# Performance work log

Hardware: AMD Instinct MI355X
Metric: run time of the kernel (lower is better)

Reference implementation:

```python
import jax, jax.numpy as jnp
import numpy as np

D_MODEL = 1024
NUM_HEADS = 16
D_K = D_MODEL // NUM_HEADS  # 64
THETA = 10000.0


def setup_inputs() -> dict:
    key = jax.random.key(0)
    k_x, k_q, k_k, k_v, k_o = jax.random.split(key, 5)
    B, S = 2, 2048
    std = (2.0 / (D_MODEL + D_MODEL)) ** 0.5
    x = jax.random.normal(k_x, (B, S, D_MODEL), dtype=jnp.float32)
    Wq = std * jax.random.truncated_normal(k_q, -3.0, 3.0, (D_MODEL, D_MODEL), dtype=jnp.float32)
    Wk = std * jax.random.truncated_normal(k_k, -3.0, 3.0, (D_MODEL, D_MODEL), dtype=jnp.float32)
    Wv = std * jax.random.truncated_normal(k_v, -3.0, 3.0, (D_MODEL, D_MODEL), dtype=jnp.float32)
    Wo = std * jax.random.truncated_normal(k_o, -3.0, 3.0, (D_MODEL, D_MODEL), dtype=jnp.float32)
    return {"x": x, "Wq": Wq, "Wk": Wk, "Wv": Wv, "Wo": Wo}


def _apply_rope(t, cos, sin):
    # t: [B, H, S, d_k]; cos/sin: [S, d_k//2] broadcast over B, H
    tr = t.reshape(*t.shape[:-1], D_K // 2, 2)
    t1, t2 = tr[..., 0], tr[..., 1]
    r1 = t1 * cos - t2 * sin
    r2 = t1 * sin + t2 * cos
    return jnp.stack([r1, r2], axis=-1).reshape(t.shape)


def reference(x, Wq, Wk, Wv, Wo):
    B, S, D = x.shape
    H, dk = NUM_HEADS, D_K
    # projections (no bias): y = x @ W.T
    Q = (x @ Wq.T).reshape(B, S, H, dk).transpose(0, 2, 1, 3)  # [B,H,S,dk]
    K = (x @ Wk.T).reshape(B, S, H, dk).transpose(0, 2, 1, 3)
    V = (x @ Wv.T).reshape(B, S, H, dk).transpose(0, 2, 1, 3)
    # RoPE angles for positions 0..S-1
    pos = jnp.arange(S, dtype=jnp.float32)[:, None]            # [S,1]
    freqs = 1.0 / (THETA ** (jnp.arange(0, dk, 2, dtype=jnp.float32) / dk))  # [dk/2]
    angles = pos * freqs[None, :]                              # [S, dk/2]
    cos, sin = jnp.cos(angles), jnp.sin(angles)
    Q = _apply_rope(Q, cos, sin)
    K = _apply_rope(K, cos, sin)
    # causal scaled dot-product attention
    scores = jnp.einsum("bhqd,bhkd->bhqk", Q, K) / jnp.sqrt(jnp.float32(dk))
    causal = jnp.tril(jnp.ones((S, S), dtype=bool))
    scores = jnp.where(causal, scores, -jnp.inf)
    probs = jax.nn.softmax(scores, axis=-1)
    attn = jnp.einsum("bhqk,bhkd->bhqd", probs, V)             # [B,H,S,dk]
    attn = attn.transpose(0, 2, 1, 3).reshape(B, S, H * dk)
    return attn @ Wo.T
```

## Files before the change

### kernel.cpp

```cpp
#include <hip/hip_runtime.h>
#include <hip/hip_bf16.h>

typedef __bf16 bf16;
typedef __bf16 bf16x8 __attribute__((ext_vector_type(8)));
typedef float f32x4 __attribute__((ext_vector_type(4)));

#define MFMA16(A, B, C) __builtin_amdgcn_mfma_f32_16x16x32_bf16((A), (B), (C), 0, 0, 0)

static __device__ __forceinline__ void gload16(const bf16* g, bf16* l) {
    __builtin_amdgcn_global_load_lds((const __attribute__((address_space(1))) void*)g,
                                     (__attribute__((address_space(3))) void*)l, 16, 0, 0);
}

__global__ void detect_kernel(const void* w, int* flag) {
    float v = (float)((const bf16*)w)[threadIdx.x];
    unsigned long long bad = __ballot(!(fabsf(v) < 1.0f));
    if (threadIdx.x == 0) *flag = bad ? 1 : 0;
}

__global__ __launch_bounds__(256) void convert_all(const void* x, const void* w0,
                                                   const void* w1, const void* w2,
                                                   const void* w3, bf16* xb, bf16* b0,
                                                   bf16* b1, bf16* b2, bf16* b3,
                                                   const int* flagp) {
    if (*flagp == 0) return;
    int id = (blockIdx.x * 256 + threadIdx.x) * 4;
    const int XN = 1 << 22;
    const float* src;
    bf16* dst;
    int off;
    if (id < XN) {
        src = (const float*)x; dst = xb; off = id;
    } else {
        int r = id - XN;
        int wi = r >> 20;
        off = r & ((1 << 20) - 1);
        src = (const float*)(wi == 0 ? w0 : wi == 1 ? w1 : wi == 2 ? w2 : w3);
        dst = (wi == 0 ? b0 : wi == 1 ? b1 : wi == 2 ? b2 : b3);
    }
    float4 v = *(const float4*)(src + off);
    bf16 o[4] = {(bf16)v.x, (bf16)v.y, (bf16)v.z, (bf16)v.w};
    *(uint2*)(dst + off) = *(uint2*)o;
}

template <int MODE>
__global__ __launch_bounds__(256) void gemm128(const void* rawA, const bf16* convA,
                                               const void* rW0, const bf16* cW0,
                                               const void* rW1, const bf16* cW1,
                                               const void* rW2, const bf16* cW2,
                                               bf16* Qo, bf16* Ko, bf16* Vt,
                                               void* Cout, const int* flagp) {
    const int K = 1024;
    __shared__ __attribute__((aligned(16))) bf16 lsA[128 * 64];
    __shared__ __attribute__((aligned(16))) bf16 lsB[128 * 64];
    const int flag = *flagp;
    const bf16* A = flag ? convA : (const bf16*)rawA;
    int tensor, n0;
    const bf16* W;
    if (MODE == 0) {
        tensor = blockIdx.x >> 3;
        n0 = (blockIdx.x & 7) * 128;
        W = tensor == 0 ? (flag ? cW0 : (const bf16*)rW0)
          : tensor == 1 ? (flag ? cW1 : (const bf16*)rW1)
                        : (flag ? cW2 : (const bf16*)rW2);
    } else {
        tensor = 0;
        n0 = blockIdx.x * 128;
        W = flag ? cW0 : (const bf16*)rW0;
    }
    const int t = threadIdx.x;
    const int m0 = blockIdx.y * 128;
    const int w = t >> 6, lane = t & 63;
    const int wr = w >> 1, wc = w & 1;
    const int llo = lane & 15, quad = lane >> 4;

    const int srow = t >> 3;
    const int sc = (t & 7) ^ (srow & 7);
    const bf16* Ab = A + (size_t)(m0 + srow) * K + sc * 8;
    const bf16* Wb = W + (size_t)(n0 + srow) * K + sc * 8;
    bf16* lA = &lsA[t * 8];
    bf16* lB = &lsB[t * 8];

    f32x4 acc[4][4] = {};

    for (int k0 = 0; k0 < K; k0 += 64) {
#pragma unroll
        for (int j = 0; j < 4; ++j) gload16(Ab + (size_t)j * 32 * K + k0, lA + j * 2048);
#pragma unroll
        for (int j = 0; j < 4; ++j) gload16(Wb + (size_t)j * 32 * K + k0, lB + j * 2048);
        __syncthreads();
#pragma unroll
        for (int kc = 0; kc < 2; ++kc) {
            bf16x8 a[4], bb[4];
            const int g = kc * 4 + quad;
#pragma unroll
            for (int mi = 0; mi < 4; ++mi) {
                int r = wr * 64 + mi * 16 + llo;
                a[mi] = *(const bf16x8*)&lsA[r * 64 + ((g ^ (r & 7)) * 8)];
            }
#pragma unroll
            for (int ni = 0; ni < 4; ++ni) {
                int r = wc * 64 + ni * 16 + llo;
                bb[ni] = *(const bf16x8*)&lsB[r * 64 + ((g ^ (r & 7)) * 8)];
            }
#pragma unroll
            for (int mi = 0; mi < 4; ++mi)
#pragma unroll
                for (int ni = 0; ni < 4; ++ni)
                    acc[mi][ni] = MFMA16(a[mi], bb[ni], acc[mi][ni]);
        }
        __syncthreads();
    }

#pragma unroll
    for (int mi = 0; mi < 4; ++mi)
#pragma unroll
        for (int ni = 0; ni < 4; ++ni)
#pragma unroll
            for (int r = 0; r < 4; ++r) {
                int row = m0 + wr * 64 + mi * 16 + quad * 4 + r;
                int col = n0 + wc * 64 + ni * 16 + llo;
                float v = acc[mi][ni][r];
                if (MODE == 1) {
                    if (flag)
                        ((float*)Cout)[(size_t)row * 1024 + col] = v;
                    else
                        ((bf16*)Cout)[(size_t)row * 1024 + col] = (bf16)v;
                } else if (tensor == 2) {
                    int b = row >> 11, s = row & 2047;
                    Vt[((size_t)b * 1024 + col) * 2048 + s] = (bf16)v;
                } else {
                    int d = col & 63, s = row & 2047;
                    float partner = __shfl_xor(v, 1);
                    float freq = exp2f((float)(d >> 1) * -0.4152410118609203f);
                    float rev = (float)s * freq * 0.15915494309189535f;
                    rev -= floorf(rev);
                    float sn = __builtin_amdgcn_sinf(rev);
                    float cs = __builtin_amdgcn_cosf(rev);
                    float outv = v * cs + partner * sn * ((d & 1) ? 1.0f : -1.0f);
                    bf16* dst = (tensor == 0) ? Qo : Ko;
                    dst[(size_t)row * 1024 + col] = (bf16)outv;
                }
            }
}

__global__ __launch_bounds__(256) void attn_kernel(const bf16* __restrict__ Q,
                                                   const bf16* __restrict__ Kr,
                                                   const bf16* __restrict__ Vt,
                                                   bf16* __restrict__ O) {
    __shared__ __attribute__((aligned(16))) bf16 lsK[64 * 64];
    __shared__ __attribute__((aligned(16))) bf16 lsV[64 * 64];
    __shared__ __attribute__((aligned(16))) bf16 lsP[4][32 * 72];
    const int blk = blockIdx.x;
    const int ib = 15 - (blk >> 5);
    const int bh = blk & 31;
    const int b = bh >> 4, h = bh & 15;
    const int t = threadIdx.x, w = t >> 6, lane = t & 63;
    const int llo = lane & 15, quad = lane >> 4;
    const int Q0 = ib * 128, q0w = Q0 + w * 32;

    bf16x8 aQ[2][2];
#pragma unroll
    for (int qi = 0; qi < 2; ++qi) {
        const size_t qb = ((size_t)(b * 2048 + q0w + qi * 16 + llo)) * 1024 + h * 64 + quad * 8;
        aQ[qi][0] = *(const bf16x8*)&Q[qb];
        aQ[qi][1] = *(const bf16x8*)&Q[qb + 32];
    }

    f32x4 o[2][4] = {};
    float lpart[2] = {0.f, 0.f};
    const float SC = 0.18033688011112042f;
    const int qlane0 = q0w + llo;

    const int srow8 = lane >> 3;
    const int sc = (lane & 7) ^ srow8;
    const int nch = 2 * ib + 2;

    for (int tt = 0; tt < nch; ++tt) {
        const int kv0 = tt * 64;
#pragma unroll
        for (int jj = 0; jj < 2; ++jj) {
            int seg = w + jj * 4;
            int rowk = seg * 8 + srow8;
            gload16(&Kr[((size_t)(b * 2048 + kv0 + rowk)) * 1024 + h * 64 + sc * 8],
                    &lsK[seg * 512 + lane * 8]);
            gload16(&Vt[((size_t)(b * 1024 + h * 64 + rowk)) * 2048 + kv0 + sc * 8],
                    &lsV[seg * 512 + lane * 8]);
        }
        __syncthreads();

        if (kv0 <= q0w + 31) {
            const bool need_mask = (kv0 + 63 >= q0w);
#pragma unroll
            for (int qi = 0; qi < 2; ++qi) {
                const int q = qlane0 + qi * 16;
#pragma unroll
                for (int half = 0; half < 4; ++half) {
                    int rk = half * 16 + llo;
                    bf16x8 k0 = *(const bf16x8*)&lsK[rk * 64 + ((quad ^ (rk & 7)) * 8)];
                    bf16x8 k1 = *(const bf16x8*)&lsK[rk * 64 + (((quad + 4) ^ (rk & 7)) * 8)];
                    f32x4 z = {};
                    z = MFMA16(k0, aQ[qi][0], z);
                    z = MFMA16(k1, aQ[qi][1], z);
                    union { bf16 hh[4]; uint2 u; } pk;
                    if (need_mask) {
                        int kvb = kv0 + half * 16 + quad * 4;
#pragma unroll
                        for (int r = 0; r < 4; ++r) {
                            float e = (kvb + r <= q) ? z[r] * SC : -INFINITY;
                            float p = exp2f(e);
                            lpart[qi] += p;
                            pk.hh[r] = (bf16)p;
                        }
                    } else {
#pragma unroll
                        for (int r = 0; r < 4; ++r) {
                            float p = exp2f(z[r] * SC);
                            lpart[qi] += p;
                            pk.hh[r] = (bf16)p;
                        }
                    }
                    *(uint2*)&lsP[w][(qi * 16 + llo) * 72 + half * 16 + quad * 4] = pk.u;
                }
            }
            __builtin_amdgcn_wave_barrier();
#pragma unroll
            for (int qi = 0; qi < 2; ++qi)
#pragma unroll
                for (int kc = 0; kc < 2; ++kc) {
                    bf16x8 aP =
                        *(const bf16x8*)&lsP[w][(qi * 16 + llo) * 72 + kc * 32 + quad * 8];
#pragma unroll
                    for (int g = 0; g < 4; ++g) {
                        int rv = g * 16 + llo;
                        int cg = kc * 4 + quad;
                        bf16x8 bV = *(const bf16x8*)&lsV[rv * 64 + ((cg ^ (rv & 7)) * 8)];
                        o[qi][g] = MFMA16(aP, bV, o[qi][g]);
                    }
                }
            __builtin_amdgcn_wave_barrier();
        }
        __syncthreads();
    }

    float lfull[2];
#pragma unroll
    for (int qi = 0; qi < 2; ++qi) {
        float l = lpart[qi];
        l += __shfl_xor(l, 16);
        l += __shfl_xor(l, 32);
        lfull[qi] = l;
    }
#pragma unroll
    for (int qi = 0; qi < 2; ++qi)
#pragma unroll
        for (int r = 0; r < 4; ++r) {
            float l = __shfl(lfull[qi], (lane & 48) | (quad * 4 + r));
            float inv = 1.f / l;
            int q = q0w + qi * 16 + quad * 4 + r;
            size_t ob = ((size_t)(b * 2048 + q)) * 1024 + h * 64;
#pragma unroll
            for (int g = 0; g < 4; ++g)
                O[ob + g * 16 + llo] = (bf16)(o[qi][g][r] * inv);
        }
}

extern "C" void kernel_launch(void* const* d_in, const int* in_sizes, int n_in,
                              void* d_out, int out_size, void* d_ws, size_t ws_size,
                              hipStream_t stream) {
    const size_t TN = (size_t)4096 * 1024;

    int* flag = (int*)d_ws;
    bf16* Q = (bf16*)((char*)d_ws + 256);
    bf16* Kb = Q + TN;
    bf16* Vt = Kb + TN;
    bf16* xb = Vt + TN;
    bf16* Wb0 = xb + TN;
    bf16* Wb1 = Wb0 + TN / 4;
    bf16* Wb2 = Wb1 + TN / 4;
    bf16* Wb3 = Wb2 + TN / 4;
    bf16* AO = Q;

    detect_kernel<<<1, 64, 0, stream>>>(d_in[1], flag);
    convert_all<<<8192, 256, 0, stream>>>(d_in[0], d_in[1], d_in[2], d_in[3], d_in[4],
                                          xb, Wb0, Wb1, Wb2, Wb3, flag);

    gemm128<0><<<dim3(24, 32), 256, 0, stream>>>(d_in[0], xb, d_in[1], Wb0, d_in[2],
                                                 Wb1, d_in[3], Wb2, Q, Kb, Vt, nullptr,
                                                 flag);

    attn_kernel<<<512, 256, 0, stream>>>(Q, Kb, Vt, AO);

    gemm128<1><<<dim3(8, 32), 256, 0, stream>>>(AO, AO, d_in[4], Wb3, nullptr, nullptr,
                                                nullptr, nullptr, nullptr, nullptr,
                                                nullptr, d_out, flag);
}
```

Measured before the change: 227.9 us.

## Double-buffer attention K/V tiles, rebalance schedule, and split output GEMM into narrower tiles

The attention kernel now double-buffers K and V tiles in LDS, prefetching the next chunk while computing the current one, so one barrier per iteration is dropped. K and V fragments are hoisted into registers, and the P buffer uses an XOR swizzle instead of padding. Query blocks are interleaved heavy and light to balance causal work. The output projection gets its own 128x64-tile kernel, giving 512 blocks instead of 256 for better CU occupancy, at the cost of more LDS per attention block and higher register pressure.

After: 215.4 us. -5.5%, faster.

```diff
diff --git a/kernel.cpp b/kernel.cpp
--- a/kernel.cpp
+++ b/kernel.cpp
@@ -43,31 +43,22 @@
     *(uint2*)(dst + off) = *(uint2*)o;
 }
 
-template <int MODE>
-__global__ __launch_bounds__(256) void gemm128(const void* rawA, const bf16* convA,
-                                               const void* rW0, const bf16* cW0,
-                                               const void* rW1, const bf16* cW1,
-                                               const void* rW2, const bf16* cW2,
-                                               bf16* Qo, bf16* Ko, bf16* Vt,
-                                               void* Cout, const int* flagp) {
+__global__ __launch_bounds__(256) void gemm_qkv(const void* rawA, const bf16* convA,
+                                                const void* rW0, const bf16* cW0,
+                                                const void* rW1, const bf16* cW1,
+                                                const void* rW2, const bf16* cW2,
+                                                bf16* Qo, bf16* Ko, bf16* Vt,
+                                                const int* flagp) {
     const int K = 1024;
     __shared__ __attribute__((aligned(16))) bf16 lsA[128 * 64];
     __shared__ __attribute__((aligned(16))) bf16 lsB[128 * 64];
     const int flag = *flagp;
     const bf16* A = flag ? convA : (const bf16*)rawA;
-    int tensor, n0;
-    const bf16* W;
-    if (MODE == 0) {
-        tensor = blockIdx.x >> 3;
-        n0 = (blockIdx.x & 7) * 128;
-        W = tensor == 0 ? (flag ? cW0 : (const bf16*)rW0)
-          : tensor == 1 ? (flag ? cW1 : (const bf16*)rW1)
-                        : (flag ? cW2 : (const bf16*)rW2);
-    } else {
-        tensor = 0;
-        n0 = blockIdx.x * 128;
-        W = flag ? cW0 : (const bf16*)rW0;
-    }
+    const int tensor = blockIdx.x >> 3;
+    const int n0 = (blockIdx.x & 7) * 128;
+    const bf16* W = tensor == 0 ? (flag ? cW0 : (const bf16*)rW0)
+                  : tensor == 1 ? (flag ? cW1 : (const bf16*)rW1)
+                                : (flag ? cW2 : (const bf16*)rW2);
     const int t = threadIdx.x;
     const int m0 = blockIdx.y * 128;
     const int w = t >> 6, lane = t & 63;
@@ -121,12 +112,7 @@
                 int row = m0 + wr * 64 + mi * 16 + quad * 4 + r;
                 int col = n0 + wc * 64 + ni * 16 + llo;
                 float v = acc[mi][ni][r];
-                if (MODE == 1) {
-                    if (flag)
-                        ((float*)Cout)[(size_t)row * 1024 + col] = v;
-                    else
-                        ((bf16*)Cout)[(size_t)row * 1024 + col] = (bf16)v;
-                } else if (tensor == 2) {
+                if (tensor == 2) {
                     int b = row >> 11, s = row & 2047;
                     Vt[((size_t)b * 1024 + col) * 2048 + s] = (bf16)v;
                 } else {
@@ -144,25 +130,94 @@
             }
 }
 
-__global__ __launch_bounds__(256) void attn_kernel(const bf16* __restrict__ Q,
-                                                   const bf16* __restrict__ Kr,
-                                                   const bf16* __restrict__ Vt,
-                                                   bf16* __restrict__ O) {
-    __shared__ __attribute__((aligned(16))) bf16 lsK[64 * 64];
-    __shared__ __attribute__((aligned(16))) bf16 lsV[64 * 64];
-    __shared__ __attribute__((aligned(16))) bf16 lsP[4][32 * 72];
+__global__ __launch_bounds__(256) void gemm_out(const bf16* A, const void* rW,
+                                                const bf16* cW, void* Cout,
+                                                const int* flagp) {
+    const int K = 1024;
+    __shared__ __attribute__((aligned(16))) bf16 lsA[128 * 64];
+    __shared__ __attribute__((aligned(16))) bf16 lsB[64 * 64];
+    const int flag = *flagp;
+    const bf16* W = flag ? cW : (const bf16*)rW;
+    const int t = threadIdx.x;
+    const int m0 = blockIdx.y * 128;
+    const int n0 = blockIdx.x * 64;
+    const int w = t >> 6, lane = t & 63;
+    const int llo = lane & 15, quad = lane >> 4;
+    const int srow = t >> 3;
+    const int sc = (t & 7) ^ (srow & 7);
+    const bf16* Ab = A + (size_t)(m0 + srow) * K + sc * 8;
+    const bf16* Wb = W + (size_t)(n0 + srow) * K + sc * 8;
+    bf16* lA = &lsA[t * 8];
+    bf16* lB = &lsB[t * 8];
+
+    f32x4 acc[2][4] = {};
+
+    for (int k0 = 0; k0 < K; k0 += 64) {
+#pragma unroll
+        for (int j = 0; j < 4; ++j) gload16(Ab + (size_t)j * 32 * K + k0, lA + j * 2048);
+#pragma unroll
+        for (int j = 0; j < 2; ++j) gload16(Wb + (size_t)j * 32 * K + k0, lB + j * 2048);
+        __syncthreads();
+#pragma unroll
+        for (int kc = 0; kc < 2; ++kc) {
+            bf16x8 a[2], bb[4];
+            const int g = kc * 4 + quad;
+#pragma unroll
+            for (int mi = 0; mi < 2; ++mi) {
+                int r = w * 32 + mi * 16 + llo;
+                a[mi] = *(const bf16x8*)&lsA[r * 64 + ((g ^ (r & 7)) * 8)];
+            }
+#pragma unroll
+            for (int ni = 0; ni < 4; ++ni) {
+                int r = ni * 16 + llo;
+                bb[ni] = *(const bf16x8*)&lsB[r * 64 + ((g ^ (r & 7)) * 8)];
+            }
+#pragma unroll
+            for (int mi = 0; mi < 2; ++mi)
+#pragma unroll
+                for (int ni = 0; ni < 4; ++ni)
+                    acc[mi][ni] = MFMA16(a[mi], bb[ni], acc[mi][ni]);
+        }
+        __syncthreads();
+    }
+
+#pragma unroll
+    for (int mi = 0; mi < 2; ++mi)
+#pragma unroll
+        for (int ni = 0; ni < 4; ++ni)
+#pragma unroll
+            for (int r = 0; r < 4; ++r) {
+                int row = m0 + w * 32 + mi * 16 + quad * 4 + r;
+                int col = n0 + ni * 16 + llo;
+                float v = acc[mi][ni][r];
+                if (flag)
+                    ((float*)Cout)[(size_t)row * 1024 + col] = v;
+                else
+                    ((bf16*)Cout)[(size_t)row * 1024 + col] = (bf16)v;
+            }
+}
+
+__global__ __launch_bounds__(256, 2) void attn_kernel(const bf16* __restrict__ Q,
+                                                      const bf16* __restrict__ Kr,
+                                                      const bf16* __restrict__ Vt,
+                                                      bf16* __restrict__ O) {
+    __shared__ __attribute__((aligned(16))) bf16 lsK[2][64 * 64];
+    __shared__ __attribute__((aligned(16))) bf16 lsV[2][64 * 64];
+    __shared__ __attribute__((aligned(16))) bf16 lsP[4][32 * 64];
     const int blk = blockIdx.x;
-    const int ib = 15 - (blk >> 5);
+    const int u = blk >> 5;
+    const int ib = (u < 8) ? (15 - u) : (u - 8);
     const int bh = blk & 31;
     const int b = bh >> 4, h = bh & 15;
     const int t = threadIdx.x, w = t >> 6, lane = t & 63;
     const int llo = lane & 15, quad = lane >> 4;
-    const int Q0 = ib * 128, q0w = Q0 + w * 32;
+    const int q0w = ib * 128 + w * 32;
 
     bf16x8 aQ[2][2];
 #pragma unroll
     for (int qi = 0; qi < 2; ++qi) {
-        const size_t qb = ((size_t)(b * 2048 + q0w + qi * 16 + llo)) * 1024 + h * 64 + quad * 8;
+        const size_t qb =
+            ((size_t)(b * 2048 + q0w + qi * 16 + llo)) * 1024 + h * 64 + quad * 8;
         aQ[qi][0] = *(const bf16x8*)&Q[qb];
         aQ[qi][1] = *(const bf16x8*)&Q[qb + 32];
     }
@@ -176,33 +231,58 @@
     const int sc = (lane & 7) ^ srow8;
     const int nch = 2 * ib + 2;
 
-    for (int tt = 0; tt < nch; ++tt) {
+    auto stage = [&](int tt, int buf) {
         const int kv0 = tt * 64;
 #pragma unroll
         for (int jj = 0; jj < 2; ++jj) {
             int seg = w + jj * 4;
             int rowk = seg * 8 + srow8;
             gload16(&Kr[((size_t)(b * 2048 + kv0 + rowk)) * 1024 + h * 64 + sc * 8],
-                    &lsK[seg * 512 + lane * 8]);
+                    &lsK[buf][seg * 512 + lane * 8]);
             gload16(&Vt[((size_t)(b * 1024 + h * 64 + rowk)) * 2048 + kv0 + sc * 8],
-                    &lsV[seg * 512 + lane * 8]);
-        }
-        __syncthreads();
+                    &lsV[buf][seg * 512 + lane * 8]);
+        }
+    };
+
+    stage(0, 0);
+
+    for (int tt = 0; tt < nch; ++tt) {
+        const int cur = tt & 1;
+        const int kv0 = tt * 64;
+        __syncthreads();
+        if (tt + 1 < nch) stage(tt + 1, cur ^ 1);
 
         if (kv0 <= q0w + 31) {
+            bf16x8 kf[4][2];
+#pragma unroll
+            for (int half = 0; half < 4; ++half) {
+                int rk = half * 16 + llo;
+                kf[half][0] = *(const bf16x8*)&lsK[cur][rk * 64 + ((quad ^ (rk & 7)) * 8)];
+                kf[half][1] =
+                    *(const bf16x8*)&lsK[cur][rk * 64 + (((quad + 4) ^ (rk & 7)) * 8)];
+            }
+            bf16x8 vf[2][4];
+#pragma unroll
+            for (int kc = 0; kc < 2; ++kc)
+#pragma unroll
+                for (int g = 0; g < 4; ++g) {
+                    int rv = g * 16 + llo;
+                    int cg = kc * 4 + quad;
+                    vf[kc][g] =
+                        *(const bf16x8*)&lsV[cur][rv * 64 + ((cg ^ (rv & 7)) * 8)];
+                }
+
             const bool need_mask = (kv0 + 63 >= q0w);
 #pragma unroll
             for (int qi = 0; qi < 2; ++qi) {
                 const int q = qlane0 + qi * 16;
+                const int prow = qi * 16 + llo;
 #pragma unroll
                 for (int half = 0; half < 4; ++half) {
-                    int rk = half * 16 + llo;
-                    bf16x8 k0 = *(const bf16x8*)&lsK[rk * 64 + ((quad ^ (rk & 7)) * 8)];
-                    bf16x8 k1 = *(const bf16x8*)&lsK[rk * 64 + (((quad + 4) ^ (rk & 7)) * 8)];
                     f32x4 z = {};
-                    z = MFMA16(k0, aQ[qi][0], z);
-                    z = MFMA16(k1, aQ[qi][1], z);
-                    union { bf16 hh[4]; uint2 u; } pk;
+                    z = MFMA16(kf[half][0], aQ[qi][0], z);
+                    z = MFMA16(kf[half][1], aQ[qi][1], z);
+                    union { bf16 hh[4]; uint2 uu; } pk;
                     if (need_mask) {
                         int kvb = kv0 + half * 16 + quad * 4;
 #pragma unroll
@@ -220,27 +300,26 @@
                             pk.hh[r] = (bf16)p;
                         }
                     }
-                    *(uint2*)&lsP[w][(qi * 16 + llo) * 72 + half * 16 + quad * 4] = pk.u;
+                    int cw = 2 * half + (quad >> 1);
+                    *(uint2*)&lsP[w][prow * 64 + ((cw ^ (llo & 7)) * 8) + (quad & 1) * 4] =
+                        pk.uu;
                 }
             }
             __builtin_amdgcn_wave_barrier();
 #pragma unroll
-            for (int qi = 0; qi < 2; ++qi)
+            for (int qi = 0; qi < 2; ++qi) {
+                const int prow = qi * 16 + llo;
 #pragma unroll
                 for (int kc = 0; kc < 2; ++kc) {
+                    int cr = 4 * kc + quad;
                     bf16x8 aP =
-                        *(const bf16x8*)&lsP[w][(qi * 16 + llo) * 72 + kc * 32 + quad * 8];
-#pragma unroll
-                    for (int g = 0; g < 4; ++g) {
-                        int rv = g * 16 + llo;
-                        int cg = kc * 4 + quad;
-                        bf16x8 bV = *(const bf16x8*)&lsV[rv * 64 + ((cg ^ (rv & 7)) * 8)];
-                        o[qi][g] = MFMA16(aP, bV, o[qi][g]);
-                    }
+                        *(const bf16x8*)&lsP[w][prow * 64 + ((cr ^ (llo & 7)) * 8)];
+#pragma unroll
+                    for (int g = 0; g < 4; ++g) o[qi][g] = MFMA16(aP, vf[kc][g], o[qi][g]);
                 }
+            }
             __builtin_amdgcn_wave_barrier();
         }
-        __syncthreads();
     }
 
     float lfull[2];
@@ -285,13 +364,10 @@
     convert_all<<<8192, 256, 0, stream>>>(d_in[0], d_in[1], d_in[2], d_in[3], d_in[4],
                                           xb, Wb0, Wb1, Wb2, Wb3, flag);
 
-    gemm128<0><<<dim3(24, 32), 256, 0, stream>>>(d_in[0], xb, d_in[1], Wb0, d_in[2],
-                                                 Wb1, d_in[3], Wb2, Q, Kb, Vt, nullptr,
-                                                 flag);
+    gemm_qkv<<<dim3(24, 32), 256, 0, stream>>>(d_in[0], xb, d_in[1], Wb0, d_in[2], Wb1,
+                                               d_in[3], Wb2, Q, Kb, Vt, flag);
 
     attn_kernel<<<512, 256, 0, stream>>>(Q, Kb, Vt, AO);
 
-    gemm128<1><<<dim3(8, 32), 256, 0, stream>>>(AO, AO, d_in[4], Wb3, nullptr, nullptr,
-                                                nullptr, nullptr, nullptr, nullptr,
-                                                nullptr, d_out, flag);
-}
+    gemm_out<<<dim3(16, 32), 256, 0, stream>>>(AO, d_in[4], Wb3, d_out, flag);
+}
```

## Double-buffer LDS in GEMM and attention, shrink GEMM tiles, balance causal blocks

Applied to the files above, without the earlier changes.

The GEMM moves to 128x64 tiles with 128 threads and a 32-wide K step, and double-buffers LDS so the next tile's global-to-LDS load overlaps the current tile's MFMAs. The attention kernel double-buffers K/V tiles, drops the trailing syncthreads, hoists K and V fragment reads out of the inner loops, swizzles the P scratch, and reorders query blocks so long and short causal rows interleave. The aim is to hide global load latency, raise occupancy and balance work across CUs. In exchange it holds more registers for the hoisted fragments and uses twice the shared memory in attention.

After: 224.3 us. About the same (-1.5%).

```diff
diff --git a/kernel.cpp b/kernel.cpp
--- a/kernel.cpp
+++ b/kernel.cpp
@@ -44,72 +44,82 @@
 }
 
 template <int MODE>
-__global__ __launch_bounds__(256) void gemm128(const void* rawA, const bf16* convA,
-                                               const void* rW0, const bf16* cW0,
-                                               const void* rW1, const bf16* cW1,
-                                               const void* rW2, const bf16* cW2,
-                                               bf16* Qo, bf16* Ko, bf16* Vt,
-                                               void* Cout, const int* flagp) {
+__global__ __launch_bounds__(128, 3) void gemm_nt(const void* rawA, const bf16* convA,
+                                                  const void* rW0, const bf16* cW0,
+                                                  const void* rW1, const bf16* cW1,
+                                                  const void* rW2, const bf16* cW2,
+                                                  bf16* Qo, bf16* Ko, bf16* Vt,
+                                                  void* Cout, const int* flagp) {
     const int K = 1024;
-    __shared__ __attribute__((aligned(16))) bf16 lsA[128 * 64];
-    __shared__ __attribute__((aligned(16))) bf16 lsB[128 * 64];
+    __shared__ __attribute__((aligned(16))) bf16 lsA[2][128 * 32];
+    __shared__ __attribute__((aligned(16))) bf16 lsB[2][64 * 32];
     const int flag = *flagp;
     const bf16* A = flag ? convA : (const bf16*)rawA;
     int tensor, n0;
     const bf16* W;
     if (MODE == 0) {
-        tensor = blockIdx.x >> 3;
-        n0 = (blockIdx.x & 7) * 128;
+        tensor = blockIdx.x >> 4;
+        n0 = (blockIdx.x & 15) * 64;
         W = tensor == 0 ? (flag ? cW0 : (const bf16*)rW0)
           : tensor == 1 ? (flag ? cW1 : (const bf16*)rW1)
                         : (flag ? cW2 : (const bf16*)rW2);
     } else {
         tensor = 0;
-        n0 = blockIdx.x * 128;
+        n0 = blockIdx.x * 64;
         W = flag ? cW0 : (const bf16*)rW0;
     }
     const int t = threadIdx.x;
     const int m0 = blockIdx.y * 128;
     const int w = t >> 6, lane = t & 63;
-    const int wr = w >> 1, wc = w & 1;
     const int llo = lane & 15, quad = lane >> 4;
-
-    const int srow = t >> 3;
-    const int sc = (t & 7) ^ (srow & 7);
-    const bf16* Ab = A + (size_t)(m0 + srow) * K + sc * 8;
-    const bf16* Wb = W + (size_t)(n0 + srow) * K + sc * 8;
-    bf16* lA = &lsA[t * 8];
-    bf16* lB = &lsB[t * 8];
+    const int sel = (llo >> 1) & 3;
 
     f32x4 acc[4][4] = {};
 
-    for (int k0 = 0; k0 < K; k0 += 64) {
-#pragma unroll
-        for (int j = 0; j < 4; ++j) gload16(Ab + (size_t)j * 32 * K + k0, lA + j * 2048);
-#pragma unroll
-        for (int j = 0; j < 4; ++j) gload16(Wb + (size_t)j * 32 * K + k0, lB + j * 2048);
+    auto stage = [&](int k0, int buf) {
+#pragma unroll
+        for (int j = 0; j < 4; ++j) {
+            int c = j * 128 + t;
+            int row = c >> 2, pos = c & 3;
+            int g = pos ^ ((row >> 1) & 3);
+            gload16(A + (size_t)(m0 + row) * K + k0 + g * 8, &lsA[buf][c * 8]);
+        }
+#pragma unroll
+        for (int j = 0; j < 2; ++j) {
+            int c = j * 128 + t;
+            int row = c >> 2, pos = c & 3;
+            int g = pos ^ ((row >> 1) & 3);
+            gload16(W + (size_t)(n0 + row) * K + k0 + g * 8, &lsB[buf][c * 8]);
+        }
+    };
+
+    auto compute = [&](int buf) {
+        bf16x8 a[4], bb[4];
+#pragma unroll
+        for (int mi = 0; mi < 4; ++mi) {
+            int r = w * 64 + mi * 16 + llo;
+            a[mi] = *(const bf16x8*)&lsA[buf][r * 32 + ((quad ^ sel) * 8)];
+        }
+#pragma unroll
+        for (int ni = 0; ni < 4; ++ni) {
+            int r = ni * 16 + llo;
+            bb[ni] = *(const bf16x8*)&lsB[buf][r * 32 + ((quad ^ sel) * 8)];
+        }
+#pragma unroll
+        for (int mi = 0; mi < 4; ++mi)
+#pragma unroll
+            for (int ni = 0; ni < 4; ++ni)
+                acc[mi][ni] = MFMA16(a[mi], bb[ni], acc[mi][ni]);
+    };
+
+    stage(0, 0);
+    for (int it = 0; it < 32; it += 2) {
         __syncthreads();
-#pragma unroll
-        for (int kc = 0; kc < 2; ++kc) {
-            bf16x8 a[4], bb[4];
-            const int g = kc * 4 + quad;
-#pragma unroll
-            for (int mi = 0; mi < 4; ++mi) {
-                int r = wr * 64 + mi * 16 + llo;
-                a[mi] = *(const bf16x8*)&lsA[r * 64 + ((g ^ (r & 7)) * 8)];
-            }
-#pragma unroll
-            for (int ni = 0; ni < 4; ++ni) {
-                int r = wc * 64 + ni * 16 + llo;
-                bb[ni] = *(const bf16x8*)&lsB[r * 64 + ((g ^ (r & 7)) * 8)];
-            }
-#pragma unroll
-            for (int mi = 0; mi < 4; ++mi)
-#pragma unroll
-                for (int ni = 0; ni < 4; ++ni)
-                    acc[mi][ni] = MFMA16(a[mi], bb[ni], acc[mi][ni]);
-        }
+        stage((it + 1) * 32, 1);
+        compute(0);
         __syncthreads();
+        if (it + 2 < 32) stage((it + 2) * 32, 0);
+        compute(1);
     }
 
 #pragma unroll
@@ -118,8 +128,8 @@
         for (int ni = 0; ni < 4; ++ni)
 #pragma unroll
             for (int r = 0; r < 4; ++r) {
-                int row = m0 + wr * 64 + mi * 16 + quad * 4 + r;
-                int col = n0 + wc * 64 + ni * 16 + llo;
+                int row = m0 + w * 64 + mi * 16 + quad * 4 + r;
+                int col = n0 + ni * 16 + llo;
                 float v = acc[mi][ni][r];
                 if (MODE == 1) {
                     if (flag)
@@ -144,25 +154,27 @@
             }
 }
 
-__global__ __launch_bounds__(256) void attn_kernel(const bf16* __restrict__ Q,
-                                                   const bf16* __restrict__ Kr,
-                                                   const bf16* __restrict__ Vt,
-                                                   bf16* __restrict__ O) {
-    __shared__ __attribute__((aligned(16))) bf16 lsK[64 * 64];
-    __shared__ __attribute__((aligned(16))) bf16 lsV[64 * 64];
-    __shared__ __attribute__((aligned(16))) bf16 lsP[4][32 * 72];
+__global__ __launch_bounds__(256, 2) void attn_kernel(const bf16* __restrict__ Q,
+                                                      const bf16* __restrict__ Kr,
+                                                      const bf16* __restrict__ Vt,
+                                                      bf16* __restrict__ O) {
+    __shared__ __attribute__((aligned(16))) bf16 lsK[2][64 * 64];
+    __shared__ __attribute__((aligned(16))) bf16 lsV[2][64 * 64];
+    __shared__ __attribute__((aligned(16))) bf16 lsP[4][32 * 64];
     const int blk = blockIdx.x;
-    const int ib = 15 - (blk >> 5);
+    const int u = blk >> 5;
+    const int ib = (u < 8) ? (15 - u) : (u - 8);
     const int bh = blk & 31;
     const int b = bh >> 4, h = bh & 15;
     const int t = threadIdx.x, w = t >> 6, lane = t & 63;
     const int llo = lane & 15, quad = lane >> 4;
-    const int Q0 = ib * 128, q0w = Q0 + w * 32;
+    const int q0w = ib * 128 + w * 32;
 
     bf16x8 aQ[2][2];
 #pragma unroll
     for (int qi = 0; qi < 2; ++qi) {
-        const size_t qb = ((size_t)(b * 2048 + q0w + qi * 16 + llo)) * 1024 + h * 64 + quad * 8;
+        const size_t qb =
+            ((size_t)(b * 2048 + q0w + qi * 16 + llo)) * 1024 + h * 64 + quad * 8;
         aQ[qi][0] = *(const bf16x8*)&Q[qb];
         aQ[qi][1] = *(const bf16x8*)&Q[qb + 32];
     }
@@ -176,33 +188,58 @@
     const int sc = (lane & 7) ^ srow8;
     const int nch = 2 * ib + 2;
 
-    for (int tt = 0; tt < nch; ++tt) {
+    auto stage = [&](int tt, int buf) {
         const int kv0 = tt * 64;
 #pragma unroll
         for (int jj = 0; jj < 2; ++jj) {
             int seg = w + jj * 4;
             int rowk = seg * 8 + srow8;
             gload16(&Kr[((size_t)(b * 2048 + kv0 + rowk)) * 1024 + h * 64 + sc * 8],
-                    &lsK[seg * 512 + lane * 8]);
+                    &lsK[buf][seg * 512 + lane * 8]);
             gload16(&Vt[((size_t)(b * 1024 + h * 64 + rowk)) * 2048 + kv0 + sc * 8],
-                    &lsV[seg * 512 + lane * 8]);
-        }
+                    &lsV[buf][seg * 512 + lane * 8]);
+        }
+    };
+
+    stage(0, 0);
+
+    for (int tt = 0; tt < nch; ++tt) {
+        const int cur = tt & 1;
+        const int kv0 = tt * 64;
         __syncthreads();
+        if (tt + 1 < nch) stage(tt + 1, cur ^ 1);
 
         if (kv0 <= q0w + 31) {
+            bf16x8 kf[4][2];
+#pragma unroll
+            for (int half = 0; half < 4; ++half) {
+                int rk = half * 16 + llo;
+                kf[half][0] = *(const bf16x8*)&lsK[cur][rk * 64 + ((quad ^ (rk & 7)) * 8)];
+                kf[half][1] =
+                    *(const bf16x8*)&lsK[cur][rk * 64 + (((quad + 4) ^ (rk & 7)) * 8)];
+            }
+            bf16x8 vf[2][4];
+#pragma unroll
+            for (int kc = 0; kc < 2; ++kc)
+#pragma unroll
+                for (int g = 0; g < 4; ++g) {
+                    int rv = g * 16 + llo;
+                    int cg = kc * 4 + quad;
+                    vf[kc][g] =
+                        *(const bf16x8*)&lsV[cur][rv * 64 + ((cg ^ (rv & 7)) * 8)];
+                }
+
             const bool need_mask = (kv0 + 63 >= q0w);
 #pragma unroll
             for (int qi = 0; qi < 2; ++qi) {
                 const int q = qlane0 + qi * 16;
+                const int prow = qi * 16 + llo;
 #pragma unroll
                 for (int half = 0; half < 4; ++half) {
-                    int rk = half * 16 + llo;
-                    bf16x8 k0 = *(const bf16x8*)&lsK[rk * 64 + ((quad ^ (rk & 7)) * 8)];
-                    bf16x8 k1 = *(const bf16x8*)&lsK[rk * 64 + (((quad + 4) ^ (rk & 7)) * 8)];
                     f32x4 z = {};
-                    z = MFMA16(k0, aQ[qi][0], z);
-                    z = MFMA16(k1, aQ[qi][1], z);
-                    union { bf16 hh[4]; uint2 u; } pk;
+                    z = MFMA16(kf[half][0], aQ[qi][0], z);
+                    z = MFMA16(kf[half][1], aQ[qi][1], z);
+                    union { bf16 hh[4]; uint2 uu; } pk;
                     if (need_mask) {
                         int kvb = kv0 + half * 16 + quad * 4;
 #pragma unroll
@@ -220,27 +257,26 @@
                             pk.hh[r] = (bf16)p;
                         }
                     }
-                    *(uint2*)&lsP[w][(qi * 16 + llo) * 72 + half * 16 + quad * 4] = pk.u;
+                    int cw = 2 * half + (quad >> 1);
+                    *(uint2*)&lsP[w][prow * 64 + ((cw ^ (llo & 7)) * 8) + (quad & 1) * 4] =
+                        pk.uu;
                 }
             }
             __builtin_amdgcn_wave_barrier();
 #pragma unroll
-            for (int qi = 0; qi < 2; ++qi)
+            for (int qi = 0; qi < 2; ++qi) {
+                const int prow = qi * 16 + llo;
 #pragma unroll
                 for (int kc = 0; kc < 2; ++kc) {
+                    int cr = 4 * kc + quad;
                     bf16x8 aP =
-                        *(const bf16x8*)&lsP[w][(qi * 16 + llo) * 72 + kc * 32 + quad * 8];
-#pragma unroll
-                    for (int g = 0; g < 4; ++g) {
-                        int rv = g * 16 + llo;
-                        int cg = kc * 4 + quad;
-                        bf16x8 bV = *(const bf16x8*)&lsV[rv * 64 + ((cg ^ (rv & 7)) * 8)];
-                        o[qi][g] = MFMA16(aP, bV, o[qi][g]);
-                    }
+                        *(const bf16x8*)&lsP[w][prow * 64 + ((cr ^ (llo & 7)) * 8)];
+#pragma unroll
+                    for (int g = 0; g < 4; ++g) o[qi][g] = MFMA16(aP, vf[kc][g], o[qi][g]);
                 }
+            }
             __builtin_amdgcn_wave_barrier();
         }
-        __syncthreads();
     }
 
     float lfull[2];
@@ -285,13 +321,13 @@
     convert_all<<<8192, 256, 0, stream>>>(d_in[0], d_in[1], d_in[2], d_in[3], d_in[4],
                                           xb, Wb0, Wb1, Wb2, Wb3, flag);
 
-    gemm128<0><<<dim3(24, 32), 256, 0, stream>>>(d_in[0], xb, d_in[1], Wb0, d_in[2],
+    gemm_nt<0><<<dim3(48, 32), 128, 0, stream>>>(d_in[0], xb, d_in[1], Wb0, d_in[2],
                                                  Wb1, d_in[3], Wb2, Q, Kb, Vt, nullptr,
                                                  flag);
 
     attn_kernel<<<512, 256, 0, stream>>>(Q, Kb, Vt, AO);
 
-    gemm128<1><<<dim3(8, 32), 256, 0, stream>>>(AO, AO, d_in[4], Wb3, nullptr, nullptr,
-                                                nullptr, nullptr, nullptr, nullptr,
-                                                nullptr, d_out, flag);
-}
+    gemm_nt<1><<<dim3(16, 32), 128, 0, stream>>>(AO, AO, d_in[4], Wb3, nullptr,
+                                                 nullptr, nullptr, nullptr, nullptr,
+                                                 nullptr, nullptr, d_out, flag);
+}
```
